# Kernel tuning notes

Measured on AMD Instinct MI355X. Metric: run time of the kernel, lower is better.

The kernel has to match this reference:

```python
import jax, jax.numpy as jnp
import numpy as np

N_IN = 10    # input_dim: x has 2**N_IN features
N_OUT = 10   # output_dim: output has 2**N_OUT features
RANK = 10
BATCH = 512
STD = 0.5


def setup_inputs() -> dict:
    key = jax.random.key(0)
    ks = jax.random.split(key, 5)
    x = jax.random.normal(ks[0], (BATCH, 2 ** N_IN), dtype=jnp.float32)
    # Stacked tensor-train cores; each core is (rank, 2, 2, rank) as in the torch module.
    input_cores = STD * jax.random.normal(ks[1], (N_IN, RANK, 2, 2, RANK), dtype=jnp.float32)
    output_cores = STD * jax.random.normal(ks[2], (N_OUT, RANK, 2, 2, RANK), dtype=jnp.float32)
    # central core is (2,)*(N_IN+N_OUT) in the original; stored here as the
    # equivalent (2**N_IN, 2**N_OUT) matrix (identical math, same memory layout).
    central_core = STD * jax.random.normal(ks[3], (2 ** N_IN, 2 ** N_OUT), dtype=jnp.float32)
    bias = STD * jax.random.normal(ks[4], (1, 2 ** N_OUT), dtype=jnp.float32)
    return {"x": x, "input_cores": input_cores, "output_cores": output_cores,
            "central_core": central_core, "bias": bias}


def reference(x, input_cores, output_cores, central_core, bias):
    # Tensor-wheel contraction with a fixed, precomputed path (replaces the
    # per-call greedy tensornetwork contractor). Exact same sum as the original.
    B = x.shape[0]
    n, r = input_cores.shape[0], input_cores.shape[1]
    m = output_cores.shape[0]

    # --- absorb x into the input-core chain ---
    # State S: (B, l0, C_acc, r_cur, Q_rem) where
    #   l0    = open left bond of input core 0 (closes the ring later)
    #   C_acc = accumulated central-core legs c_1..c_i (dim 2^i, c_1 most significant)
    #   Q_rem = remaining input bits of x (x bit 1 is most significant, matching reshape)
    S = jnp.einsum('bpq,lpcs->blcsq', x.reshape(B, 2, -1), input_cores[0])
    for i in range(1, n):
        _, l, C, rc, Q = S.shape
        S = S.reshape(B, l, C, rc, 2, Q // 2)
        S = jnp.einsum('blcrpq,rpds->blcdsq', S, input_cores[i]).reshape(B, l, 2 * C, r, Q // 2)
    S = S[..., 0]  # (B, l0, 2^n, r_n)

    # --- contract the central core over all input-side legs (dominant GEMM) ---
    U = jnp.einsum('blcr,cd->blrd', S, central_core)  # (B, l0, r_n, 2^m)

    # --- sweep through the output-core chain ---
    # State V: (B, l0, P_acc, r_cur, D_rem); P_acc accumulates free output legs
    # p_1..p_j (p_1 most significant), D_rem holds remaining central output legs.
    V = U.reshape(B, r, 1, r, 2 ** m)
    for j in range(m):
        _, l, P, rc, D = V.shape
        V = V.reshape(B, l, P, rc, 2, D // 2)
        V = jnp.einsum('blxrdq,rpds->blxpsq', V, output_cores[j]).reshape(B, l, 2 * P, r, D // 2)

    # --- close the ring: trace l0 (input core 0 left bond) with rgt_m ---
    out = jnp.einsum('blpl->bp', V[..., 0])  # (B, 2^m)
    return out + bias
```

## Files before the change

kernel.cpp:

```cpp
#include <hip/hip_runtime.h>
#include <cstdint>
#include <cstddef>


typedef __attribute__((ext_vector_type(8))) short short8;
typedef __attribute__((ext_vector_type(4))) float f32x4;

static __device__ __forceinline__ unsigned short f2bf(float f) {
  union { float f; unsigned int u; } v; v.f = f;
  unsigned int r = v.u + 0x7FFFu + ((v.u >> 16) & 1u);
  return (unsigned short)(r >> 16);
}
static __device__ __forceinline__ unsigned int pack2(float a, float b) {
  return (unsigned int)f2bf(a) | ((unsigned int)f2bf(b) << 16);
}

static __device__ __forceinline__ int shuf_in(int stg, int u, int dd) {
  if (stg == 0) return ((u >> 4) << 6) | (dd << 4) | ((u & 3) << 2) | ((u >> 2) & 3);
  if (stg == 1) return ((u >> 2) << 4) | (dd << 2) | (u & 3);
  return (u << 2) | dd;
}
static __device__ __forceinline__ int shuf_out(int stg, int u, int dd) {
  if (stg == 0) return (dd << 6) | ((u & 15) << 2) | (u >> 4);
  if (stg == 1) return ((u >> 4) << 6) | (dd << 4) | ((u & 3) << 2) | ((u >> 2) & 3);
  if (stg == 2) return ((u >> 2) << 4) | (dd << 2) | (u & 3);
  return (u << 2) | dd;
}

static __device__ __forceinline__ void mfma_stage80(
    const unsigned short* stc, const unsigned short* __restrict__ Bf,
    int w, int lane, int c15, int quad, f32x4 acc[4][3]) {
  short8 bfr[3][2];
  #pragma unroll
  for (int nt = 0; nt < 3; ++nt) {
    bfr[nt][0] = *(const short8*)&Bf[(nt * 2 + 0) * 512 + lane * 8];
    bfr[nt][1] = *(const short8*)&Bf[(nt * 2 + 1) * 512 + lane * 8];
  }
  #pragma unroll
  for (int rt = 0; rt < 4; ++rt) {
    const int rowA = w * 64 + rt * 16 + c15;
    const short8 a0 = *(const short8*)((const char*)stc + rowA * 80 + quad * 16);
    const int a1off = (quad == 0) ? rowA * 80 + 64 : 0;
    const short8 a1 = *(const short8*)((const char*)stc + a1off);
    #pragma unroll
    for (int nt = 0; nt < 3; ++nt) {
      f32x4 a = {0.f, 0.f, 0.f, 0.f};
      a = __builtin_amdgcn_mfma_f32_16x16x32_bf16(a0, bfr[nt][0], a, 0, 0, 0);
      a = __builtin_amdgcn_mfma_f32_16x16x32_bf16(a1, bfr[nt][1], a, 0, 0, 0);
      acc[rt][nt] = a;
    }
  }
}

template <int STG, bool INPUT>
static __device__ __forceinline__ void stage_writes80(
    unsigned short* dst, const f32x4 acc[4][3], int w, int quad,
    const int* ddv, const int* sv) {
  #pragma unroll
  for (int rt = 0; rt < 4; ++rt) {
    const int u = w * 16 + rt * 4 + quad;
    #pragma unroll
    for (int nt = 0; nt < 3; ++nt) {
      if (sv[nt] < 10) {
        const int dd = ddv[nt];
        const int row = INPUT ? shuf_in(STG, u, dd) : shuf_out(STG, u, dd);
        uint2 v;
        v.x = pack2(acc[rt][nt][0], acc[rt][nt][1]);
        v.y = pack2(acc[rt][nt][2], acc[rt][nt][3]);
        *(uint2*)((char*)dst + row * 80 + sv[nt] * 8) = v;
      }
    }
  }
}

__global__ __launch_bounds__(256) void k0_prep(
    const float* __restrict__ ic, const float* __restrict__ oc,
    const float* __restrict__ cc, unsigned short* __restrict__ Bt,
    float* __restrict__ c2x, unsigned short* __restrict__ bf1,
    unsigned short* __restrict__ bf3, unsigned short* __restrict__ bf3l) {
  const int t = threadIdx.x;
  const int bx = blockIdx.x;
  if (bx < 1024) {
    const int dly = bx;
    const int D = (dly & 3) * 256 + ((dly >> 2) & 3) * 64 + (dly >> 4);
    const int uC = (t >> 2) * 16 + (t & 3);
    ushort4 pk;
    pk.x = f2bf(cc[(size_t)(uC + 0) * 1024 + D]);
    pk.y = f2bf(cc[(size_t)(uC + 4) * 1024 + D]);
    pk.z = f2bf(cc[(size_t)(uC + 8) * 1024 + D]);
    pk.w = f2bf(cc[(size_t)(uC + 12) * 1024 + D]);
    *(ushort4*)&Bt[(size_t)dly * 1024 + 4 * t] = pk;
  } else if (bx == 1024) {
    for (int idx = t; idx < 1600; idx += 256) {
      int L = idx / 160, rem = idx - L * 160;
      int w = rem / 40, r2 = rem - w * 40;
      int pi = r2 / 10, s = r2 - pi * 10;
      int p1 = pi >> 1, p2 = pi & 1, c1 = w >> 1, c2v = w & 1;
      float a = 0.f;
      for (int r1 = 0; r1 < 10; ++r1)
        a += ic[L * 40 + p1 * 20 + c1 * 10 + r1] *
             ic[400 + r1 * 40 + p2 * 20 + c2v * 10 + s];
      c2x[idx] = a;
    }
  } else if (bx == 1025) {
    for (int idx = t; idx < 12288; idx += 256) {
      int j = idx & 7, lane = (idx >> 3) & 63, kc = (idx >> 9) & 1;
      int g2 = idx >> 10, stg = g2 / 3, nt = g2 - stg * 3;
      int c15 = lane & 15, quad = lane >> 4;
      int n = nt * 16 + c15, dd = n / 12, s = n - dd * 12;
      int k = kc * 32 + quad * 8 + j, c = k >> 2, pi = k & 3;
      float v = 0.f;
      if (k < 40 && s < 10) {
        int p1 = pi >> 1, p2 = pi & 1, d1 = dd >> 1, d2 = dd & 1;
        const float* A = ic + (2 * stg + 2) * 400;
        const float* B = ic + (2 * stg + 3) * 400;
        for (int tt = 0; tt < 10; ++tt)
          v += A[c * 40 + p1 * 20 + d1 * 10 + tt] *
               B[tt * 40 + p2 * 20 + d2 * 10 + s];
      }
      bf1[idx] = f2bf(v);
    }
  } else if (bx == 1026) {
    for (int idx = t; idx < 12288; idx += 256) {
      int j = idx & 7, lane = (idx >> 3) & 63, kc = (idx >> 9) & 1;
      int g2 = idx >> 10, stg = g2 / 3, nt = g2 - stg * 3;
      int c15 = lane & 15, quad = lane >> 4;
      int n = nt * 16 + c15, dd = n / 12, s = n - dd * 12;
      int k = kc * 32 + quad * 8 + j, c = k >> 2, pi = k & 3;
      float v = 0.f;
      if (k < 40 && s < 10) {
        int d1 = pi >> 1, d2 = pi & 1, p1 = dd >> 1, p2 = dd & 1;
        const float* A = oc + (2 * stg) * 400;
        const float* B = oc + (2 * stg + 1) * 400;
        for (int tt = 0; tt < 10; ++tt)
          v += A[c * 40 + p1 * 20 + d1 * 10 + tt] *
               B[tt * 40 + p2 * 20 + d2 * 10 + s];
      }
      bf3[idx] = f2bf(v);
    }
  } else {
    for (int idx = t; idx < 10240; idx += 256) {
      int j = idx & 7, lane = (idx >> 3) & 63, kc = (idx >> 9) & 1, L = idx >> 10;
      int c15 = lane & 15, quad = lane >> 4;
      int k = kc * 32 + quad * 8 + j, c = k >> 2, pi = k & 3;
      float v = 0.f;
      if (k < 40 && c15 < 4) {
        int dd = c15, d1 = pi >> 1, d2 = pi & 1, p1 = dd >> 1, p2 = dd & 1;
        for (int tt = 0; tt < 10; ++tt)
          v += oc[8 * 400 + c * 40 + p1 * 20 + d1 * 10 + tt] *
               oc[9 * 400 + tt * 40 + p2 * 20 + d2 * 10 + L];
      }
      bf3l[idx] = f2bf(v);
    }
  }
}

__global__ __launch_bounds__(256, 4) void k1_insweep(
    const float* __restrict__ x, const float* __restrict__ c2x,
    const unsigned short* __restrict__ bf1, unsigned short* __restrict__ S) {
  __shared__ __align__(16) unsigned short st[20480];
  const int t = threadIdx.x, bx = blockIdx.x;
  const int b = bx / 10, L = bx - b * 10;
  const int lane = t & 63, w = t >> 6;
  const int c15 = lane & 15, quad = lane >> 4;
  int ddv[3], sv[3];
  #pragma unroll
  for (int nt = 0; nt < 3; ++nt) {
    int n = nt * 16 + c15; ddv[nt] = n / 12; sv[nt] = n - ddv[nt] * 12;
  }
  unsigned short* bufA = st;
  unsigned short* bufB = st + 10240;
  {
    const float* xb = x + (size_t)b * 1024;
    const float* C2 = c2x + L * 160 + w * 40;
    float accx[4][10];
    #pragma unroll
    for (int g = 0; g < 4; ++g)
      #pragma unroll
      for (int s = 0; s < 10; ++s) accx[g][s] = 0.f;
    #pragma unroll
    for (int pi = 0; pi < 4; ++pi) {
      float xv[4];
      #pragma unroll
      for (int g = 0; g < 4; ++g) xv[g] = xb[pi * 256 + g * 64 + lane];
      #pragma unroll
      for (int s = 0; s < 10; ++s) {
        const float bv = C2[pi * 10 + s];
        #pragma unroll
        for (int g = 0; g < 4; ++g) accx[g][s] = fmaf(xv[g], bv, accx[g][s]);
      }
    }
    const int row = w * 64 + c15 * 4 + quad;
    #pragma unroll
    for (int s = 0; s < 10; ++s) {
      uint2 v;
      v.x = pack2(accx[0][s], accx[1][s]);
      v.y = pack2(accx[2][s], accx[3][s]);
      *(uint2*)((char*)bufA + row * 80 + s * 8) = v;
    }
  }
  __syncthreads();
  f32x4 acc[4][3];
  mfma_stage80(bufA, bf1 + 0 * 3072, w, lane, c15, quad, acc);
  stage_writes80<0, true>(bufB, acc, w, quad, ddv, sv);
  __syncthreads();
  mfma_stage80(bufB, bf1 + 1 * 3072, w, lane, c15, quad, acc);
  stage_writes80<1, true>(bufA, acc, w, quad, ddv, sv);
  __syncthreads();
  mfma_stage80(bufA, bf1 + 2 * 3072, w, lane, c15, quad, acc);
  stage_writes80<2, true>(bufB, acc, w, quad, ddv, sv);
  __syncthreads();
  mfma_stage80(bufB, bf1 + 3 * 3072, w, lane, c15, quad, acc);
  #pragma unroll
  for (int rt = 0; rt < 4; ++rt) {
    const int u = w * 16 + rt * 4 + quad;
    #pragma unroll
    for (int nt = 0; nt < 3; ++nt) {
      if (sv[nt] < 10) {
        uint2 v;
        v.x = pack2(acc[rt][nt][0], acc[rt][nt][1]);
        v.y = pack2(acc[rt][nt][2], acc[rt][nt][3]);
        *(uint2*)&S[((size_t)(bx * 10 + sv[nt])) * 1024 + u * 16 + ddv[nt] * 4] = v;
      }
    }
  }
}


#define K2_STAGE6(SLOT)                                                        \
  {                                                                            \
    char* lb = ldsb + (SLOT) * 24576 + w * 6144;                               \
    _Pragma("unroll")                                                          \
    for (int i = 0; i < 6; ++i) {                                              \
      __builtin_amdgcn_global_load_lds(                                        \
          (const __attribute__((address_space(1))) void*)(gsrc[i]),            \
          (__attribute__((address_space(3))) void*)(lb + (i << 10)), 16, 0, 0);\
      gsrc[i] += 32;                            \
    }                                                                          \
  }

#define K2_PHASE(RSLOT, SSLOT, DO_STAGE, VMCNT_ASM, DO_SYNC)                   \
  {                                                                            \
    const char* rb = ldsb + (RSLOT) * 24576;                                   \
    short8 afr[8], bfr[4];                                                     \
    _Pragma("unroll")                                                          \
    for (int mt = 0; mt < 8; ++mt)                                             \
      afr[mt] = *(const short8*)(rb + ((arow0 + (mt << 4)) << 6) + aswz);      \
    _Pragma("unroll")                                                          \
    for (int nt = 0; nt < 4; ++nt)                                             \
      bfr[nt] = *(const short8*)(rb + 16384 + ((brow0 + (nt << 4)) << 6) + aswz);\
    if (DO_STAGE) K2_STAGE6(SSLOT)                                             \
    __builtin_amdgcn_s_setprio(1);                                             \
    _Pragma("unroll")                                                          \
    for (int mt = 0; mt < 8; ++mt)                                             \
      _Pragma("unroll")                                                        \
      for (int nt = 0; nt < 4; ++nt)                                           \
        acc[mt][nt] = __builtin_amdgcn_mfma_f32_16x16x32_bf16(                 \
            afr[mt], bfr[nt], acc[mt][nt], 0, 0, 0);                           \
    __builtin_amdgcn_s_setprio(0);                                             \
    if (DO_SYNC) {                                                             \
      VMCNT_ASM;                                \
      __builtin_amdgcn_s_barrier();             \
      __builtin_amdgcn_sched_barrier(0);                                       \
    }                                                                          \
  }

#define K2_VM6 asm volatile("s_waitcnt vmcnt(6)" ::: "memory")
#define K2_VM0 asm volatile("s_waitcnt vmcnt(0)" ::: "memory")

__global__ __launch_bounds__(256, 2) void k2_gemm(
    const unsigned short* __restrict__ A,
    const unsigned short* __restrict__ B,
    unsigned short* __restrict__ U2a,
    unsigned short* __restrict__ U2b) {
  __shared__ __align__(16) char ldsb[73728];
  const int tid = threadIdx.x, bx = blockIdx.x;
  const int bid = (bx & 7) * 200 + (bx >> 3);
  const int bm = bid & 3, bn = bid >> 2;
  const int Mtile0 = bm << 8, Ntile0 = bn << 7;
  const int w = tid >> 6, lane = tid & 63;
  const int c15 = lane & 15, quad = lane >> 4;
  const int wm = w >> 1, wn = w & 1;

  const int arow0 = (wm << 7) + c15;
  const int brow0 = (wn << 6) + c15;
  const int aswz = ((quad ^ ((c15 >> 1) & 3)) << 4);

  const unsigned short* gsrc[6];
  #pragma unroll
  for (int i = 0; i < 6; ++i) {
    const int rowc = w * 96 + i * 16;
    const int row = rowc + (lane >> 2);
    const unsigned short* g = (rowc < 256)
        ? (A + ((size_t)(Mtile0 + row) << 10))
        : (B + ((size_t)(Ntile0 + row - 256) << 10));
    gsrc[i] = g + (((lane & 3) ^ ((lane >> 3) & 3)) << 3);
  }

  f32x4 acc[8][4];
  #pragma unroll
  for (int i = 0; i < 8; ++i)
    #pragma unroll
    for (int j = 0; j < 4; ++j) acc[i][j] = (f32x4){0.f, 0.f, 0.f, 0.f};

  K2_STAGE6(0)
  K2_STAGE6(1)
  K2_VM6;
  __builtin_amdgcn_s_barrier();
  __builtin_amdgcn_sched_barrier(0);

  #pragma unroll 1
  for (int it = 0; it < 10; ++it) {
    K2_PHASE(0, 2, true, K2_VM6, true)
    K2_PHASE(1, 0, true, K2_VM6, true)
    K2_PHASE(2, 1, true, K2_VM6, true)
  }
  K2_PHASE(0, 2, false, K2_VM0, true)
  K2_PHASE(1, 2, false, (void)0, false)

  const int col0 = Ntile0 + (wn << 6) + c15;
  const int rowb = Mtile0 + (wm << 7);
  #pragma unroll
  for (int nt = 0; nt < 4; ++nt) {
    const int n = col0 + (nt << 4);
    const int bl = n / 10;
    const int r = n - bl * 10;
    char* dst = (r < 8)
        ? (char*)U2a + (size_t)bl * 16384 + (size_t)r * 8
        : (char*)U2b + (size_t)bl * 4096 + (size_t)(r - 8) * 8;
    const int rbs = (r < 8) ? 64 : 16;
    #pragma unroll
    for (int mt = 0; mt < 8; ++mt) {
      const int mp = (rowb + (mt << 4) + (quad << 2)) >> 2;
      uint2 v;
      v.x = pack2(acc[mt][nt][0], acc[mt][nt][1]);
      v.y = pack2(acc[mt][nt][2], acc[mt][nt][3]);
      *(uint2*)(dst + (size_t)mp * rbs) = v;
    }
  }
}

__global__ __launch_bounds__(256, 4) void k3_outsweep(
    const unsigned short* __restrict__ U2a, const unsigned short* __restrict__ U2b,
    const unsigned short* __restrict__ bf3, const unsigned short* __restrict__ bf3l,
    const float* __restrict__ bias, float* __restrict__ out) {
  __shared__ __align__(16) unsigned short st[20480];
  const int t = threadIdx.x, bx = blockIdx.x;
  const int b = bx / 10, L = bx - b * 10;
  const int lane = t & 63, w = t >> 6;
  const int c15 = lane & 15, quad = lane >> 4;
  int ddv[3], sv[3];
  #pragma unroll
  for (int nt = 0; nt < 3; ++nt) {
    int n = nt * 16 + c15; ddv[nt] = n / 12; sv[nt] = n - ddv[nt] * 12;
  }
  unsigned short* bufA = st;
  unsigned short* bufB = st + 10240;
  f32x4 acc[4][3];
  {
    short8 bfr[3][2];
    #pragma unroll
    for (int nt = 0; nt < 3; ++nt) {
      bfr[nt][0] = *(const short8*)&bf3[(nt * 2 + 0) * 512 + lane * 8];
      bfr[nt][1] = *(const short8*)&bf3[(nt * 2 + 1) * 512 + lane * 8];
    }
    const char* Ua = (const char*)U2a + (size_t)bx * 16384;
    const char* Ub = (const char*)U2b + (size_t)bx * 4096;
    #pragma unroll
    for (int rt = 0; rt < 4; ++rt) {
      const int m = w * 64 + rt * 16 + c15;
      const short8 a0 = *(const short8*)(Ua + m * 64 + quad * 16);
      const short8 a1 = *(const short8*)(Ub + m * 16);
      #pragma unroll
      for (int nt = 0; nt < 3; ++nt) {
        f32x4 a = {0.f, 0.f, 0.f, 0.f};
        a = __builtin_amdgcn_mfma_f32_16x16x32_bf16(a0, bfr[nt][0], a, 0, 0, 0);
        a = __builtin_amdgcn_mfma_f32_16x16x32_bf16(a1, bfr[nt][1], a, 0, 0, 0);
        acc[rt][nt] = a;
      }
    }
    stage_writes80<0, false>(bufA, acc, w, quad, ddv, sv);
  }
  __syncthreads();
  mfma_stage80(bufA, bf3 + 1 * 3072, w, lane, c15, quad, acc);
  stage_writes80<1, false>(bufB, acc, w, quad, ddv, sv);
  __syncthreads();
  mfma_stage80(bufB, bf3 + 2 * 3072, w, lane, c15, quad, acc);
  stage_writes80<2, false>(bufA, acc, w, quad, ddv, sv);
  __syncthreads();
  mfma_stage80(bufA, bf3 + 3 * 3072, w, lane, c15, quad, acc);
  stage_writes80<3, false>(bufB, acc, w, quad, ddv, sv);
  __syncthreads();
  {
    const unsigned short* Bf = bf3l + L * 1024;
    const short8 b0 = *(const short8*)&Bf[lane * 8];
    const short8 b1 = *(const short8*)&Bf[512 + lane * 8];
    #pragma unroll
    for (int rt = 0; rt < 4; ++rt) {
      const int rowA = w * 64 + rt * 16 + c15;
      const short8 a0 = *(const short8*)((const char*)bufB + rowA * 80 + quad * 16);
      const int a1off = (quad == 0) ? rowA * 80 + 64 : 0;
      const short8 a1 = *(const short8*)((const char*)bufB + a1off);
      f32x4 a = {0.f, 0.f, 0.f, 0.f};
      a = __builtin_amdgcn_mfma_f32_16x16x32_bf16(a0, b0, a, 0, 0, 0);
      a = __builtin_amdgcn_mfma_f32_16x16x32_bf16(a1, b1, a, 0, 0, 0);
      if (c15 < 4) {
        const int u = w * 16 + rt * 4 + quad;
        #pragma unroll
        for (int i = 0; i < 4; ++i) {
          const int oidx = u * 16 + i * 4 + c15;
          float v = a[i];
          if (L == 0) v += bias[oidx];
          atomicAdd(&out[(size_t)b * 1024 + oidx], v);
        }
      }
    }
  }
}

extern "C" void kernel_launch(void* const* d_in, const int* in_sizes, int n_in,
                              void* d_out, int out_size, void* d_ws, size_t ws_size,
                              hipStream_t stream) {
  (void)in_sizes; (void)n_in; (void)ws_size;
  const float* x    = (const float*)d_in[0];
  const float* ic   = (const float*)d_in[1];
  const float* oc   = (const float*)d_in[2];
  const float* cc   = (const float*)d_in[3];
  const float* bias = (const float*)d_in[4];
  float* out = (float*)d_out;

  char* ws = (char*)d_ws;
  unsigned short* S    = (unsigned short*)(ws);
  unsigned short* U2a  = (unsigned short*)(ws + 104857600);
  unsigned short* U2b  = (unsigned short*)(ws + 188743680);
  unsigned short* Bt   = (unsigned short*)(ws + 209715200);
  float*          c2x  = (float*)(ws + 211812352);
  unsigned short* bf1  = (unsigned short*)(ws + 211818752);
  unsigned short* bf3  = (unsigned short*)(ws + 211843328);
  unsigned short* bf3l = (unsigned short*)(ws + 211867904);

  hipMemsetAsync(d_out, 0, (size_t)out_size * sizeof(float), stream);
  k0_prep<<<1028, 256, 0, stream>>>(ic, oc, cc, Bt, c2x, bf1, bf3, bf3l);
  k1_insweep<<<5120, 256, 0, stream>>>(x, c2x, bf1, S);
  k2_gemm<<<1600, 256, 0, stream>>>(Bt, S, U2a, U2b);
  k3_outsweep<<<5120, 256, 0, stream>>>(U2a, U2b, bf3, bf3l, bias, out);
}
```

Measured before the change: 339.3 us.

## Double-buffer LDS fragment reads in GEMM mainloop and use immediate global offsets

The GEMM mainloop now reads the next stage's A/B fragments from LDS into a second register set while the MFMAs for the current stage run on the first set. It also folds the per-stage global pointer increments into immediate offsets, bumping pointers only once per six stages. The aim is to hide LDS read latency behind MFMA work and cut address arithmetic. The cost is twice the fragment registers, which raises pressure under the 2-blocks-per-CU launch bound and could cause spills or lower occupancy.

```diff
diff --git a/kernel.cpp b/kernel.cpp
--- a/kernel.cpp
+++ b/kernel.cpp
@@ -227,46 +227,51 @@
 }
 
 
-#define K2_STAGE6(SLOT)                                                        \
+#define K2_STAGE6(SSLOT, IMMS)                                                 \
   {                                                                            \
-    char* lb = ldsb + (SLOT) * 24576 + w * 6144;                               \
+    char* lb = ldsb + (SSLOT) * 24576 + w * 6144;                              \
     _Pragma("unroll")                                                          \
-    for (int i = 0; i < 6; ++i) {                                              \
+    for (int i = 0; i < 6; ++i)                                                \
       __builtin_amdgcn_global_load_lds(                                        \
-          (const __attribute__((address_space(1))) void*)(gsrc[i]),            \
+          (const __attribute__((address_space(1))) void*)(gsrc[i] + (IMMS)),   \
           (__attribute__((address_space(3))) void*)(lb + (i << 10)), 16, 0, 0);\
-      gsrc[i] += 32;                            \
-    }                                                                          \
-  }
-
-#define K2_PHASE(RSLOT, SSLOT, DO_STAGE, VMCNT_ASM, DO_SYNC)                   \
+  }
+
+#define K2_READF(DSTF, RSLOTN)                                                 \
   {                                                                            \
-    const char* rb = ldsb + (RSLOT) * 24576;                                   \
-    short8 afr[8], bfr[4];                                                     \
+    const char* rbn = ldsb + (RSLOTN) * 24576;                                 \
     _Pragma("unroll")                                                          \
     for (int mt = 0; mt < 8; ++mt)                                             \
-      afr[mt] = *(const short8*)(rb + ((arow0 + (mt << 4)) << 6) + aswz);      \
+      DSTF[mt] = *(const short8*)(rbn + ((arow0 + (mt << 4)) << 6) + aswz);    \
     _Pragma("unroll")                                                          \
     for (int nt = 0; nt < 4; ++nt)                                             \
-      bfr[nt] = *(const short8*)(rb + 16384 + ((brow0 + (nt << 4)) << 6) + aswz);\
-    if (DO_STAGE) K2_STAGE6(SSLOT)                                             \
+      DSTF[8 + nt] =                                                           \
+          *(const short8*)(rbn + 16384 + ((brow0 + (nt << 4)) << 6) + aswz);   \
+  }
+
+#define K2_PHASE(CURF, NXTF, RSLOTN, SSLOT, IMMS, DO_READ, DO_STAGE, VMCNT_ASM, DO_SYNC) \
+  {                                                                            \
+    if (DO_READ) K2_READF(NXTF, RSLOTN)                                        \
+    if (DO_STAGE) K2_STAGE6(SSLOT, IMMS)                                       \
     __builtin_amdgcn_s_setprio(1);                                             \
     _Pragma("unroll")                                                          \
     for (int mt = 0; mt < 8; ++mt)                                             \
       _Pragma("unroll")                                                        \
       for (int nt = 0; nt < 4; ++nt)                                           \
         acc[mt][nt] = __builtin_amdgcn_mfma_f32_16x16x32_bf16(                 \
-            afr[mt], bfr[nt], acc[mt][nt], 0, 0, 0);                           \
+            CURF[mt], CURF[8 + nt], acc[mt][nt], 0, 0, 0);                     \
     __builtin_amdgcn_s_setprio(0);                                             \
     if (DO_SYNC) {                                                             \
-      VMCNT_ASM;                                \
-      __builtin_amdgcn_s_barrier();             \
+      asm volatile("s_waitcnt lgkmcnt(0)" ::: "memory");                       \
+      VMCNT_ASM;                                                               \
+      __builtin_amdgcn_s_barrier();                                            \
       __builtin_amdgcn_sched_barrier(0);                                       \
     }                                                                          \
   }
 
 #define K2_VM6 asm volatile("s_waitcnt vmcnt(6)" ::: "memory")
 #define K2_VM0 asm volatile("s_waitcnt vmcnt(0)" ::: "memory")
+#define K2_NOVM (void)0
 
 __global__ __launch_bounds__(256, 2) void k2_gemm(
     const unsigned short* __restrict__ A,
@@ -303,20 +308,38 @@
     #pragma unroll
     for (int j = 0; j < 4; ++j) acc[i][j] = (f32x4){0.f, 0.f, 0.f, 0.f};
 
-  K2_STAGE6(0)
-  K2_STAGE6(1)
+  short8 F0[12], F1[12];
+
+  K2_STAGE6(0, 0)
+  K2_STAGE6(1, 32)
+  K2_VM6;
+  __builtin_amdgcn_s_barrier();
+  K2_READF(F0, 0)
+  K2_STAGE6(2, 64)
+  asm volatile("s_waitcnt lgkmcnt(0)" ::: "memory");
   K2_VM6;
   __builtin_amdgcn_s_barrier();
   __builtin_amdgcn_sched_barrier(0);
 
   #pragma unroll 1
-  for (int it = 0; it < 10; ++it) {
-    K2_PHASE(0, 2, true, K2_VM6, true)
-    K2_PHASE(1, 0, true, K2_VM6, true)
-    K2_PHASE(2, 1, true, K2_VM6, true)
-  }
-  K2_PHASE(0, 2, false, K2_VM0, true)
-  K2_PHASE(1, 2, false, (void)0, false)
+  for (int it = 0; it < 4; ++it) {
+    K2_PHASE(F0, F1, 1, 0,  96, true, true, K2_VM6, true)
+    K2_PHASE(F1, F0, 2, 1, 128, true, true, K2_VM6, true)
+    K2_PHASE(F0, F1, 0, 2, 160, true, true, K2_VM6, true)
+    K2_PHASE(F1, F0, 1, 0, 192, true, true, K2_VM6, true)
+    K2_PHASE(F0, F1, 2, 1, 224, true, true, K2_VM6, true)
+    K2_PHASE(F1, F0, 0, 2, 256, true, true, K2_VM6, true)
+    #pragma unroll
+    for (int i = 0; i < 6; ++i) gsrc[i] += 192;
+  }
+  K2_PHASE(F0, F1, 1, 0,  96, true, true,  K2_VM6, true)
+  K2_PHASE(F1, F0, 2, 1, 128, true, true,  K2_VM6, true)
+  K2_PHASE(F0, F1, 0, 2, 160, true, true,  K2_VM6, true)
+  K2_PHASE(F1, F0, 1, 0, 192, true, true,  K2_VM6, true)
+  K2_PHASE(F0, F1, 2, 1, 224, true, true,  K2_VM6, true)
+  K2_PHASE(F1, F0, 0, 0, 0,   true, false, K2_VM0, true)
+  K2_PHASE(F0, F1, 1, 0, 0,   true, false, K2_NOVM, false)
+  K2_PHASE(F1, F0, 0, 0, 0,   false, false, K2_NOVM, false)
 
   const int col0 = Ntile0 + (wn << 6) + c15;
   const int rowb = Mtile0 + (wm << 7);
```

Measured after the change: 350.0 us. 3.1% more time.
